# Kernel optimization log

Hardware: AMD Instinct MI355X
Metric: run time of the kernel (lower is better)

Reference implementation:

```python
import jax, jax.numpy as jnp
import numpy as np

D = 1024   # input_size / width
H = 1024   # hidden_size / lru_width
TW = 4     # conv1d temporal width (Griffin default)
C_GATE = 8.0


def setup_inputs() -> dict:
    key = jax.random.key(0)
    ks = jax.random.split(key, 12)
    B, T = 8, 4096
    sd = 1.0 / np.sqrt(D)
    sh = 1.0 / np.sqrt(H)
    return {
        "input_bxtxd": jax.random.normal(ks[0], (B, T, D), jnp.float32),
        "w_x": jax.random.normal(ks[1], (D, H), jnp.float32) * sd,
        "b_x": jnp.zeros((H,), jnp.float32),
        "w_y": jax.random.normal(ks[2], (D, H), jnp.float32) * sd,
        "b_y": jnp.zeros((H,), jnp.float32),
        "conv_w": jax.random.normal(ks[3], (TW, H), jnp.float32) * 0.5,
        "conv_b": jnp.zeros((H,), jnp.float32),
        "gi_w": jax.random.normal(ks[4], (H, H), jnp.float32) * sh,
        "gi_b": jnp.zeros((H,), jnp.float32),
        "ga_w": jax.random.normal(ks[5], (H, H), jnp.float32) * sh,
        "ga_b": jnp.zeros((H,), jnp.float32),
        # a_param > 0 so a = exp(-c*gate*softplus(a_param)) lies in (0,1)
        "a_param": jax.random.uniform(ks[6], (H,), jnp.float32, 2.0, 6.0),
    }


def reference(input_bxtxd, w_x, b_x, w_y, b_y, conv_w, conv_b,
              gi_w, gi_b, ga_w, ga_b, a_param):
    x = input_bxtxd                      # [B,T,D], batch_first
    B, T, _ = x.shape

    # x branch: linear_x -> causal depthwise conv1d (zero cache) -> RG-LRU
    x1 = jnp.einsum("btd,dh->bth", x, w_x) + b_x            # [B,T,H]
    xp = jnp.pad(x1, ((0, 0), (TW - 1, 0), (0, 0)))          # causal pad
    x2 = sum(conv_w[i] * xp[:, i:i + T, :] for i in range(TW)) + conv_b

    # RG-LRU gates (num_heads=1 -> full linear)
    gate_x = jax.nn.sigmoid(jnp.einsum("bth,hk->btk", x2, gi_w) + gi_b)
    gate_a = jax.nn.sigmoid(jnp.einsum("bth,hk->btk", x2, ga_w) + ga_b)
    log_a = -C_GATE * gate_a * jax.nn.softplus(a_param)      # [B,T,H]
    a = jnp.exp(log_a)
    multiplier = jnp.sqrt(jnp.maximum(1.0 - jnp.exp(2.0 * log_a), 0.0))
    # segment_pos = arange(T): reset at t == 0
    multiplier = multiplier.at[:, 0, :].set(1.0)
    a = a.at[:, 0, :].set(0.0)
    normalized_x = gate_x * x2 * multiplier                  # [B,T,H]

    # linear recurrence h_t = a_t * h_{t-1} + normalized_x_t (h_{-1}=0)
    def combine(c1, c2):
        a1, h1 = c1
        a2, h2 = c2
        return a1 * a2, h2 + a2 * h1

    _, h = jax.lax.associative_scan(combine, (a, normalized_x), axis=1)

    # y branch and output gating
    y = jax.nn.gelu(jnp.einsum("btd,dh->bth", x, w_y) + b_y, approximate=False)
    out = h * y                                              # [B,T,H]
    hn = h[:, -1, :]                                         # last state
    return out, h, hn
```

## Files before the change

### kernel.cpp

```cpp
#include <hip/hip_runtime.h>
#include <math.h>


#define B_ 8
#define T_ 4096
#define H_ 1024
#define M_ (B_ * T_)
#define NC_ 128
#define CL_ 32

typedef _Float16 half8 __attribute__((ext_vector_type(8)));
typedef _Float16 half4 __attribute__((ext_vector_type(4)));
typedef float    f32x4 __attribute__((ext_vector_type(4)));

__global__ __launch_bounds__(256) void transpose_cvt(
    const float* __restrict__ sA, const float* __restrict__ sB,
    _Float16* __restrict__ dst) {
  __shared__ float tile[32][33];
  int bn = blockIdx.x * 32;
  int bk = blockIdx.y * 32;
  const float* src = (bn < 1024) ? sA : sB;
  int nof = (bn < 1024) ? bn : bn - 1024;
  int c  = threadIdx.x & 31;
  int r0 = threadIdx.x >> 5;
#pragma unroll
  for (int i = 0; i < 4; ++i) {
    int r = r0 + i * 8;
    tile[r][c] = src[(size_t)(bk + r) * 1024 + nof + c];
  }
  __syncthreads();
#pragma unroll
  for (int i = 0; i < 4; ++i) {
    int nl = r0 + i * 8;
    dst[(size_t)(bn + nl) * 1024 + bk + c] = (_Float16)tile[c][nl];
  }
}

__global__ void prep_bias(const float* __restrict__ bx, const float* __restrict__ by,
                          const float* __restrict__ gib, const float* __restrict__ gab,
                          float* __restrict__ b1, float* __restrict__ b2) {
  int i = blockIdx.x * 1024 + threadIdx.x;
  if (i < 1024)      b1[i] = bx[i];
  else if (i < 2048) b1[i] = by[i - 1024];
  else if (i < 3072) b2[i - 2048] = gib[i - 2048];
  else               b2[i - 2048] = gab[i - 3072];
}

__global__ __launch_bounds__(256) void cvt_fp16(
    const float* __restrict__ x, _Float16* __restrict__ xh, long n4) {
  for (long i = (long)blockIdx.x * 256 + threadIdx.x; i < n4;
       i += (long)gridDim.x * 256) {
    f32x4 v = ((const f32x4*)x)[i];
    half4 h;
#pragma unroll
    for (int e = 0; e < 4; ++e) h[e] = (_Float16)v[e];
    ((half4*)xh)[i] = h;
  }
}

template <int MODE>
__global__ __launch_bounds__(256) void gemm_kernel(
    const _Float16* __restrict__ A, const _Float16* __restrict__ Bt,
    const float* __restrict__ bias, const float* __restrict__ a_param,
    _Float16* __restrict__ C) {
  __shared__ half8 AsV[512];
  __shared__ half8 BsV[512];
  const int K = 1024;
  int tid  = threadIdx.x;
  int lane = tid & 63;
  int wave = tid >> 6;
  int mtile = blockIdx.x >> 4;
  int ntile = blockIdx.x & 15;
  int m0 = mtile * 128, n0 = ntile * 128;
  int wm = wave >> 1, wn = wave & 1;

  int srow = tid >> 2;
  int skg  = tid & 3;
  const half8* Ag8 = (const half8*)(A  + (size_t)(m0 + srow) * K + skg * 8);
  const half8* Bg8 = (const half8*)(Bt + (size_t)(n0 + srow) * K + skg * 8);
  int wslot = skg * 128 + (srow ^ skg);

  f32x4 acc[4][4];
  f32x4 zero = {0.f, 0.f, 0.f, 0.f};
#pragma unroll
  for (int i = 0; i < 4; ++i)
#pragma unroll
    for (int j = 0; j < 4; ++j) acc[i][j] = zero;

  int g  = lane >> 4;
  int fa = g * 128 + wm * 64 + ((lane & 15) ^ g);
  int fb = g * 128 + wn * 64 + ((lane & 15) ^ g);

  half8 pa0 = Ag8[0], pa1 = Ag8[8192];
  half8 pb0 = Bg8[0], pb1 = Bg8[8192];

  for (int kk = 0; kk < 32; ++kk) {
    AsV[wslot]      = pa0;
    AsV[wslot + 64] = pa1;
    BsV[wslot]      = pb0;
    BsV[wslot + 64] = pb1;
    __syncthreads();
    if (kk < 31) {
      pa0 = Ag8[(kk + 1) * 4];
      pa1 = Ag8[(kk + 1) * 4 + 8192];
      pb0 = Bg8[(kk + 1) * 4];
      pb1 = Bg8[(kk + 1) * 4 + 8192];
    }
    half8 af[4], bf[4];
#pragma unroll
    for (int mi = 0; mi < 4; ++mi) af[mi] = AsV[fa + mi * 16];
#pragma unroll
    for (int ni = 0; ni < 4; ++ni) bf[ni] = BsV[fb + ni * 16];
#pragma unroll
    for (int mi = 0; mi < 4; ++mi)
#pragma unroll
      for (int ni = 0; ni < 4; ++ni)
        acc[mi][ni] = __builtin_amdgcn_mfma_f32_16x16x32_f16(
            af[mi], bf[ni], acc[mi][ni], 0, 0, 0);
    __syncthreads();
  }

  int lr = lane >> 4;
  int lc = lane & 15;
#pragma unroll
  for (int ni = 0; ni < 4; ++ni) {
    int gn = n0 + wn * 64 + ni * 16 + lc;
    float bs = bias[gn];
    float sp = 0.f;
    if (MODE == 1 && gn >= 1024) {
      float apv = a_param[gn - 1024];
      sp = log1pf(expf(apv));
    }
#pragma unroll
    for (int mi = 0; mi < 4; ++mi) {
      int gmb = m0 + wm * 64 + mi * 16 + lr * 4;
#pragma unroll
      for (int p = 0; p < 4; ++p) {
        float v = acc[mi][ni][p] + bs;
        if (MODE == 1) {
          float s = 1.f / (1.f + expf(-v));
          if (gn < 1024) {
            v = s;
          } else {
            float a = expf(-8.f * s * sp);
            if (((gmb + p) & (T_ - 1)) == 0) a = 0.f;
            v = a;
          }
        }
        C[(size_t)(gmb + p) * 2048 + gn] = (_Float16)v;
      }
    }
  }
}

__global__ __launch_bounds__(256) void conv_kernel(
    const _Float16* __restrict__ g1, const float* __restrict__ cw,
    const float* __restrict__ cb, _Float16* __restrict__ x2) {
  int idx = blockIdx.x * 256 + threadIdx.x;
  int m  = idx >> 7;
  int hb = (idx & 127) * 8;
  int t  = m & (T_ - 1);
  float acc[8];
#pragma unroll
  for (int e = 0; e < 8; ++e) acc[e] = cb[hb + e];
#pragma unroll
  for (int j = 0; j < 4; ++j) {
    if (t >= j) {
      half8 xv = *(const half8*)&g1[(size_t)(m - j) * 2048 + hb];
      const float* w = &cw[(3 - j) * 1024 + hb];
#pragma unroll
      for (int e = 0; e < 8; ++e) acc[e] += w[e] * (float)xv[e];
    }
  }
  half8 o;
#pragma unroll
  for (int e = 0; e < 8; ++e) o[e] = (_Float16)acc[e];
  *(half8*)&x2[(size_t)m * 1024 + hb] = o;
}

__global__ __launch_bounds__(256) void gatefuse_kernel(
    const _Float16* __restrict__ g2, _Float16* __restrict__ x2) {
  int idx = blockIdx.x * 256 + threadIdx.x;
  int m  = idx >> 7;
  int hb = (idx & 127) * 8;
  half8 gx = *(const half8*)&g2[(size_t)m * 2048 + hb];
  half8 av = *(const half8*)&g2[(size_t)m * 2048 + 1024 + hb];
  half8 xv = *(const half8*)&x2[(size_t)m * 1024 + hb];
  half8 o;
#pragma unroll
  for (int e = 0; e < 8; ++e) {
    float a = (float)av[e];
    float mult = sqrtf(fmaxf(1.f - a * a, 0.f));
    o[e] = (_Float16)((float)gx[e] * (float)xv[e] * mult);
  }
  *(half8*)&x2[(size_t)m * 1024 + hb] = o;
}

__global__ __launch_bounds__(128) void scan1_kernel(
    const _Float16* __restrict__ g2, const _Float16* __restrict__ nx,
    float* __restrict__ cA, float* __restrict__ cH) {
  int bid = blockIdx.x;
  int b = bid >> 7, c = bid & 127;
  int h0 = threadIdx.x * 8;
  float A[8], Hh[8];
#pragma unroll
  for (int e = 0; e < 8; ++e) { A[e] = 1.f; Hh[e] = 0.f; }
  size_t mbase = (size_t)b * T_ + (size_t)c * CL_;
  for (int i = 0; i < CL_; ++i) {
    size_t m = mbase + i;
    half8 av = *(const half8*)&g2[m * 2048 + 1024 + h0];
    half8 xv = *(const half8*)&nx[m * 1024 + h0];
#pragma unroll
    for (int e = 0; e < 8; ++e) {
      float a = (float)av[e];
      A[e] *= a;
      Hh[e] = (float)xv[e] + a * Hh[e];
    }
  }
  size_t o = (size_t)bid * 1024 + h0;
#pragma unroll
  for (int e = 0; e < 8; ++e) { cA[o + e] = A[e]; cH[o + e] = Hh[e]; }
}

__global__ void scanmid_kernel(const float* __restrict__ cA,
                               const float* __restrict__ cH,
                               float* __restrict__ carry) {
  int gidx = blockIdx.x * 256 + threadIdx.x;
  int b = gidx >> 10, h = gidx & 1023;
  float run = 0.f;
  for (int c = 0; c < NC_; ++c) {
    size_t o = ((size_t)(b * NC_ + c)) * 1024 + h;
    carry[o] = run;
    run = cH[o] + cA[o] * run;
  }
}

__global__ __launch_bounds__(128) void scan2_kernel(
    const _Float16* __restrict__ g2, const _Float16* __restrict__ nx,
    const _Float16* __restrict__ g1, const float* __restrict__ carry,
    float* __restrict__ outO, float* __restrict__ outH,
    float* __restrict__ outHn) {
  int bid = blockIdx.x;
  int b = bid >> 7, c = bid & 127;
  int h0 = threadIdx.x * 8;
  float Hh[8];
  {
    size_t o = (size_t)bid * 1024 + h0;
#pragma unroll
    for (int e = 0; e < 8; ++e) Hh[e] = carry[o + e];
  }
  size_t mbase = (size_t)b * T_ + (size_t)c * CL_;
  for (int i = 0; i < CL_; ++i) {
    size_t m = mbase + i;
    half8 av = *(const half8*)&g2[m * 2048 + 1024 + h0];
    half8 xv = *(const half8*)&nx[m * 1024 + h0];
    half8 uv = *(const half8*)&g1[m * 2048 + 1024 + h0];
    f32x4 hO[2], oO[2];
#pragma unroll
    for (int e = 0; e < 8; ++e) {
      float a = (float)av[e];
      float v = (float)xv[e] + a * Hh[e];
      Hh[e] = v;
      float u = (float)uv[e];
      float y = 0.5f * u * (1.f + erff(u * 0.70710678118654752f));
      hO[e >> 2][e & 3] = v;
      oO[e >> 2][e & 3] = v * y;
    }
    size_t ob = m * 1024 + h0;
    *(f32x4*)&outH[ob]     = hO[0];
    *(f32x4*)&outH[ob + 4] = hO[1];
    *(f32x4*)&outO[ob]     = oO[0];
    *(f32x4*)&outO[ob + 4] = oO[1];
  }
  if (c == NC_ - 1) {
    size_t o = (size_t)b * 1024 + h0;
#pragma unroll
    for (int e = 0; e < 8; ++e) outHn[o + e] = Hh[e];
  }
}

extern "C" void kernel_launch(void* const* d_in, const int* in_sizes, int n_in,
                              void* d_out, int out_size, void* d_ws,
                              size_t ws_size, hipStream_t stream) {
  const float* x   = (const float*)d_in[0];
  const float* wx  = (const float*)d_in[1];
  const float* bx  = (const float*)d_in[2];
  const float* wy  = (const float*)d_in[3];
  const float* by  = (const float*)d_in[4];
  const float* cw  = (const float*)d_in[5];
  const float* cb  = (const float*)d_in[6];
  const float* giw = (const float*)d_in[7];
  const float* gib = (const float*)d_in[8];
  const float* gaw = (const float*)d_in[9];
  const float* gab = (const float*)d_in[10];
  const float* ap  = (const float*)d_in[11];

  char* ws = (char*)d_ws;
  size_t off = 0;
  auto alloc = [&](size_t bytes) {
    char* p = ws + off;
    off += (bytes + 255) & ~(size_t)255;
    return p;
  };
  _Float16* wT1 = (_Float16*)alloc((size_t)2048 * 1024 * 2);
  _Float16* wT2 = (_Float16*)alloc((size_t)2048 * 1024 * 2);
  float*    b1  = (float*)alloc(2048 * 4);
  float*    b2  = (float*)alloc(2048 * 4);
  _Float16* xh  = (_Float16*)alloc((size_t)M_ * 1024 * 2);
  _Float16* g2e = (_Float16*)alloc((size_t)M_ * 1024 * 2);
  (void)g2e;
  _Float16* g1o = (_Float16*)alloc((size_t)M_ * 2048 * 2);
  _Float16* x2h = (_Float16*)alloc((size_t)M_ * 1024 * 2);
  float* cA  = (float*)alloc((size_t)B_ * NC_ * 1024 * 4);
  float* cH  = (float*)alloc((size_t)B_ * NC_ * 1024 * 4);
  float* cin = (float*)alloc((size_t)B_ * NC_ * 1024 * 4);
  _Float16* g2o = xh;

  float* oO  = (float*)d_out;
  float* oH  = oO + (size_t)M_ * 1024;
  float* oHn = oO + (size_t)2 * M_ * 1024;

  transpose_cvt<<<dim3(64, 32), 256, 0, stream>>>(wx, wy, wT1);
  transpose_cvt<<<dim3(64, 32), 256, 0, stream>>>(giw, gaw, wT2);
  prep_bias<<<4, 1024, 0, stream>>>(bx, by, gib, gab, b1, b2);
  cvt_fp16<<<2048, 256, 0, stream>>>(x, xh, (long)M_ * 1024 / 4);

  gemm_kernel<0><<<4096, 256, 0, stream>>>(xh, wT1, b1, nullptr, g1o);
  conv_kernel<<<16384, 256, 0, stream>>>(g1o, cw, cb, x2h);
  gemm_kernel<1><<<4096, 256, 0, stream>>>(x2h, wT2, b2, ap, g2o);
  gatefuse_kernel<<<16384, 256, 0, stream>>>(g2o, x2h);

  scan1_kernel<<<B_ * NC_, 128, 0, stream>>>(g2o, x2h, cA, cH);
  scanmid_kernel<<<32, 256, 0, stream>>>(cA, cH, cin);
  scan2_kernel<<<B_ * NC_, 128, 0, stream>>>(g2o, x2h, g1o, cin, oO, oH, oHn);
}
```

Measured before the change: 713.1 us.

## Use direct global-to-LDS loads in GEMM and fuse gate multiply into scans

```diff
diff --git a/kernel.cpp b/kernel.cpp
--- a/kernel.cpp
+++ b/kernel.cpp
@@ -12,6 +12,12 @@
 typedef _Float16 half8 __attribute__((ext_vector_type(8)));
 typedef _Float16 half4 __attribute__((ext_vector_type(4)));
 typedef float    f32x4 __attribute__((ext_vector_type(4)));
+
+__device__ __forceinline__ void load16_lds(const _Float16* g, _Float16* l) {
+  __builtin_amdgcn_global_load_lds(
+      (const __attribute__((address_space(1))) void*)g,
+      (__attribute__((address_space(3))) void*)l, 16, 0, 0);
+}
 
 __global__ __launch_bounds__(256) void transpose_cvt(
     const float* __restrict__ sA, const float* __restrict__ sB,
@@ -59,26 +65,34 @@
 }
 
 template <int MODE>
-__global__ __launch_bounds__(256) void gemm_kernel(
+__global__ __launch_bounds__(256, 2) void gemm_kernel(
     const _Float16* __restrict__ A, const _Float16* __restrict__ Bt,
     const float* __restrict__ bias, const float* __restrict__ a_param,
     _Float16* __restrict__ C) {
-  __shared__ half8 AsV[512];
-  __shared__ half8 BsV[512];
+  __shared__ _Float16 sA[128 * 32];
+  __shared__ _Float16 sB[128 * 32];
   const int K = 1024;
   int tid  = threadIdx.x;
   int lane = tid & 63;
   int wave = tid >> 6;
-  int mtile = blockIdx.x >> 4;
-  int ntile = blockIdx.x & 15;
+
+  int nb  = (int)blockIdx.x;
+  int per = (int)gridDim.x >> 3;
+  nb = (nb & 7) * per + (nb >> 3);
+  int mtile = nb >> 4;
+  int ntile = nb & 15;
   int m0 = mtile * 128, n0 = ntile * 128;
   int wm = wave >> 1, wn = wave & 1;
 
-  int srow = tid >> 2;
-  int skg  = tid & 3;
-  const half8* Ag8 = (const half8*)(A  + (size_t)(m0 + srow) * K + skg * 8);
-  const half8* Bg8 = (const half8*)(Bt + (size_t)(n0 + srow) * K + skg * 8);
-  int wslot = skg * 128 + (srow ^ skg);
+  int row0 = tid >> 2, kg0 = tid & 3;
+  const _Float16* gA0 = A  + (size_t)(m0 + row0) * K + kg0 * 8;
+  const _Float16* gA1 = gA0 + (size_t)64 * K;
+  const _Float16* gB0 = Bt + (size_t)(n0 + row0) * K + kg0 * 8;
+  const _Float16* gB1 = gB0 + (size_t)64 * K;
+  _Float16* lA0 = sA + wave * 512;
+  _Float16* lA1 = sA + 2048 + wave * 512;
+  _Float16* lB0 = sB + wave * 512;
+  _Float16* lB1 = sB + 2048 + wave * 512;
 
   f32x4 acc[4][4];
   f32x4 zero = {0.f, 0.f, 0.f, 0.f};
@@ -87,30 +101,23 @@
 #pragma unroll
     for (int j = 0; j < 4; ++j) acc[i][j] = zero;
 
-  int g  = lane >> 4;
-  int fa = g * 128 + wm * 64 + ((lane & 15) ^ g);
-  int fb = g * 128 + wn * 64 + ((lane & 15) ^ g);
-
-  half8 pa0 = Ag8[0], pa1 = Ag8[8192];
-  half8 pb0 = Bg8[0], pb1 = Bg8[8192];
+  const half8* sA8 = (const half8*)sA;
+  const half8* sB8 = (const half8*)sB;
+  int fa = (wm * 64 + (lane & 15)) * 4 + (lane >> 4);
+  int fb = (wn * 64 + (lane & 15)) * 4 + (lane >> 4);
 
   for (int kk = 0; kk < 32; ++kk) {
-    AsV[wslot]      = pa0;
-    AsV[wslot + 64] = pa1;
-    BsV[wslot]      = pb0;
-    BsV[wslot + 64] = pb1;
+    int ko = kk * 32;
+    load16_lds(gA0 + ko, lA0);
+    load16_lds(gA1 + ko, lA1);
+    load16_lds(gB0 + ko, lB0);
+    load16_lds(gB1 + ko, lB1);
     __syncthreads();
-    if (kk < 31) {
-      pa0 = Ag8[(kk + 1) * 4];
-      pa1 = Ag8[(kk + 1) * 4 + 8192];
-      pb0 = Bg8[(kk + 1) * 4];
-      pb1 = Bg8[(kk + 1) * 4 + 8192];
-    }
     half8 af[4], bf[4];
 #pragma unroll
-    for (int mi = 0; mi < 4; ++mi) af[mi] = AsV[fa + mi * 16];
-#pragma unroll
-    for (int ni = 0; ni < 4; ++ni) bf[ni] = BsV[fb + ni * 16];
+    for (int mi = 0; mi < 4; ++mi) af[mi] = sA8[fa + mi * 64];
+#pragma unroll
+    for (int ni = 0; ni < 4; ++ni) bf[ni] = sB8[fb + ni * 64];
 #pragma unroll
     for (int mi = 0; mi < 4; ++mi)
 #pragma unroll
@@ -122,32 +129,36 @@
 
   int lr = lane >> 4;
   int lc = lane & 15;
+  int   gn[4];
+  float bs[4], sp[4];
 #pragma unroll
   for (int ni = 0; ni < 4; ++ni) {
-    int gn = n0 + wn * 64 + ni * 16 + lc;
-    float bs = bias[gn];
-    float sp = 0.f;
-    if (MODE == 1 && gn >= 1024) {
-      float apv = a_param[gn - 1024];
-      sp = log1pf(expf(apv));
-    }
-#pragma unroll
-    for (int mi = 0; mi < 4; ++mi) {
-      int gmb = m0 + wm * 64 + mi * 16 + lr * 4;
-#pragma unroll
-      for (int p = 0; p < 4; ++p) {
-        float v = acc[mi][ni][p] + bs;
+    gn[ni] = n0 + wn * 64 + ni * 16 + lc;
+    bs[ni] = bias[gn[ni]];
+    sp[ni] = 0.f;
+    if (MODE == 1 && gn[ni] >= 1024)
+      sp[ni] = log1pf(expf(a_param[gn[ni] - 1024]));
+  }
+#pragma unroll
+  for (int mi = 0; mi < 4; ++mi) {
+#pragma unroll
+    for (int p = 0; p < 4; ++p) {
+      int gm = m0 + wm * 64 + mi * 16 + lr * 4 + p;
+      size_t rowb = (size_t)gm * 2048;
+#pragma unroll
+      for (int ni = 0; ni < 4; ++ni) {
+        float v = acc[mi][ni][p] + bs[ni];
         if (MODE == 1) {
           float s = 1.f / (1.f + expf(-v));
-          if (gn < 1024) {
+          if (gn[ni] < 1024) {
             v = s;
           } else {
-            float a = expf(-8.f * s * sp);
-            if (((gmb + p) & (T_ - 1)) == 0) a = 0.f;
+            float a = expf(-8.f * s * sp[ni]);
+            if ((gm & (T_ - 1)) == 0) a = 0.f;
             v = a;
           }
         }
-        C[(size_t)(gmb + p) * 2048 + gn] = (_Float16)v;
+        C[rowb + gn[ni]] = (_Float16)v;
       }
     }
   }
@@ -178,26 +189,8 @@
   *(half8*)&x2[(size_t)m * 1024 + hb] = o;
 }
 
-__global__ __launch_bounds__(256) void gatefuse_kernel(
-    const _Float16* __restrict__ g2, _Float16* __restrict__ x2) {
-  int idx = blockIdx.x * 256 + threadIdx.x;
-  int m  = idx >> 7;
-  int hb = (idx & 127) * 8;
-  half8 gx = *(const half8*)&g2[(size_t)m * 2048 + hb];
-  half8 av = *(const half8*)&g2[(size_t)m * 2048 + 1024 + hb];
-  half8 xv = *(const half8*)&x2[(size_t)m * 1024 + hb];
-  half8 o;
-#pragma unroll
-  for (int e = 0; e < 8; ++e) {
-    float a = (float)av[e];
-    float mult = sqrtf(fmaxf(1.f - a * a, 0.f));
-    o[e] = (_Float16)((float)gx[e] * (float)xv[e] * mult);
-  }
-  *(half8*)&x2[(size_t)m * 1024 + hb] = o;
-}
-
 __global__ __launch_bounds__(128) void scan1_kernel(
-    const _Float16* __restrict__ g2, const _Float16* __restrict__ nx,
+    const _Float16* __restrict__ g2, const _Float16* __restrict__ x2,
     float* __restrict__ cA, float* __restrict__ cH) {
   int bid = blockIdx.x;
   int b = bid >> 7, c = bid & 127;
@@ -208,13 +201,16 @@
   size_t mbase = (size_t)b * T_ + (size_t)c * CL_;
   for (int i = 0; i < CL_; ++i) {
     size_t m = mbase + i;
+    half8 gx = *(const half8*)&g2[m * 2048 + h0];
     half8 av = *(const half8*)&g2[m * 2048 + 1024 + h0];
-    half8 xv = *(const half8*)&nx[m * 1024 + h0];
+    half8 xv = *(const half8*)&x2[m * 1024 + h0];
 #pragma unroll
     for (int e = 0; e < 8; ++e) {
       float a = (float)av[e];
+      float mult = sqrtf(fmaxf(1.f - a * a, 0.f));
+      float nx = (float)gx[e] * (float)xv[e] * mult;
       A[e] *= a;
-      Hh[e] = (float)xv[e] + a * Hh[e];
+      Hh[e] = nx + a * Hh[e];
     }
   }
   size_t o = (size_t)bid * 1024 + h0;
@@ -236,7 +232,7 @@
 }
 
 __global__ __launch_bounds__(128) void scan2_kernel(
-    const _Float16* __restrict__ g2, const _Float16* __restrict__ nx,
+    const _Float16* __restrict__ g2, const _Float16* __restrict__ x2,
     const _Float16* __restrict__ g1, const float* __restrict__ carry,
     float* __restrict__ outO, float* __restrict__ outH,
     float* __restrict__ outHn) {
@@ -252,14 +248,17 @@
   size_t mbase = (size_t)b * T_ + (size_t)c * CL_;
   for (int i = 0; i < CL_; ++i) {
     size_t m = mbase + i;
+    half8 gx = *(const half8*)&g2[m * 2048 + h0];
     half8 av = *(const half8*)&g2[m * 2048 + 1024 + h0];
-    half8 xv = *(const half8*)&nx[m * 1024 + h0];
+    half8 xv = *(const half8*)&x2[m * 1024 + h0];
     half8 uv = *(const half8*)&g1[m * 2048 + 1024 + h0];
     f32x4 hO[2], oO[2];
 #pragma unroll
     for (int e = 0; e < 8; ++e) {
       float a = (float)av[e];
-      float v = (float)xv[e] + a * Hh[e];
+      float mult = sqrtf(fmaxf(1.f - a * a, 0.f));
+      float nx = (float)gx[e] * (float)xv[e] * mult;
+      float v = nx + a * Hh[e];
       Hh[e] = v;
       float u = (float)uv[e];
       float y = 0.5f * u * (1.f + erff(u * 0.70710678118654752f));
@@ -328,7 +327,6 @@
   gemm_kernel<0><<<4096, 256, 0, stream>>>(xh, wT1, b1, nullptr, g1o);
   conv_kernel<<<16384, 256, 0, stream>>>(g1o, cw, cb, x2h);
   gemm_kernel<1><<<4096, 256, 0, stream>>>(x2h, wT2, b2, ap, g2o);
-  gatefuse_kernel<<<16384, 256, 0, stream>>>(g2o, x2h);
 
   scan1_kernel<<<B_ * NC_, 128, 0, stream>>>(g2o, x2h, cA, cH);
   scanmid_kernel<<<32, 256, 0, stream>>>(cA, cH, cin);
```

Result: faster. 638.5 us (-10.5%).
